# Kernel tuning notes

Hardware: AMD Instinct MI355X
Metric: run time of the kernel (lower is better)

The kernel has to match this reference:

```python
import jax, jax.numpy as jnp
import numpy as np

ALPHA = -100.0


def setup_inputs() -> dict:
    key = jax.random.key(0)
    k1, k2 = jax.random.split(key)
    input_seqs = jax.random.normal(k1, (512, 1024), dtype=jnp.float32)
    shapelets = jax.random.normal(k2, (100, 50), dtype=jnp.float32)
    return {"input_seqs": input_seqs, "shapelets": shapelets}


def reference(input_seqs, shapelets):
    """Sliding-window squared distance + softmin-weighted pooling.

    input_seqs: (n, Q) float
    shapelets : (K, L) float
    returns   : (n, K) float  -- softmin-pooled normalized sq. distance
    """
    n, Q = input_seqs.shape
    K, L = shapelets.shape
    J = Q - L  # original code uses Q - L (not Q - L + 1); kept faithful

    # ||x[j:j+L]||^2 for every window via cumulative sums (no explicit loop)
    csum = jnp.concatenate(
        [jnp.zeros((n, 1), input_seqs.dtype), jnp.cumsum(input_seqs * input_seqs, axis=1)],
        axis=1,
    )  # (n, Q+1)
    sq_win = csum[:, L:L + J] - csum[:, :J]  # (n, J)

    # cross term x[j:j+L] . s_k via windowed gather + small GEMM
    idx = jnp.arange(J)[:, None] + jnp.arange(L)[None, :]  # (J, L)
    windows = input_seqs[:, idx]  # (n, J, L)
    cross = jnp.einsum("njl,kl->njk", windows, shapelets)  # (n, J, K)

    s_sq = jnp.sum(shapelets * shapelets, axis=1)  # (K,)

    # D[i, j, k] = ||x_i[j:j+L] - s_k||^2 / L
    D = (sq_win[:, :, None] - 2.0 * cross + s_sq[None, None, :]) / L  # (n, J, K)

    # subtract per-(i,k) min over window positions (as in the original)
    Dm = D - jnp.min(D, axis=1, keepdims=True)

    # softmin-weighted average: sum_j Dm * exp(alpha*Dm) / sum_j exp(alpha*Dm)
    w = jnp.exp(ALPHA * Dm)  # stable: alpha<0 and Dm>=0 after min-shift
    M = jnp.sum(Dm * w, axis=1) / jnp.sum(w, axis=1)  # (n, K)
    return M
```

## Files before the change

### kernel.cpp

```cpp
#include <hip/hip_runtime.h>


#define N_SEQ   512
#define Q_LEN   1024
#define K_SH    100
#define L_SH    50
#define J_WIN   974
#define NTILE   7
#define MTILES  61
#define ALPHA_F (-100.0f)
#define SKIP_T  0.5f
#define RINV_L  0.02f
#define PAD_SQ  4e31f

#define CPR     1064

typedef short  short8 __attribute__((ext_vector_type(8)));
typedef float  f32x4  __attribute__((ext_vector_type(4)));
typedef unsigned int uintx4 __attribute__((ext_vector_type(4)));

union V8 { short8 s; uintx4 u; };

__device__ __forceinline__ unsigned int bf16h(float f) {
    unsigned int b = __float_as_uint(f);
    return (b + 0x7FFFu + ((b >> 16) & 1u)) >> 16;
}
__device__ __forceinline__ float bf16back(unsigned int h) {
    return __uint_as_float(h << 16);
}

__device__ __forceinline__ void merge_state(float& m, float& S, float& T,
                                            float m1, float S1, float T1) {
    const float mm = fminf(m, m1);
    const float e0 = __expf(ALPHA_F * (m  - mm));
    const float e1 = __expf(ALPHA_F * (m1 - mm));
    T = (T + (m - mm) * S) * e0 + (T1 + (m1 - mm) * S1) * e1;
    S = S * e0 + S1 * e1;
    m = mm;
}

__global__ __launch_bounds__(256, 2)
void softmin_mfma_kernel(const float* __restrict__ x,
                         const float* __restrict__ sh,
                         float* __restrict__ out) {
    __shared__ __align__(16) short cp[16 * CPR];
    __shared__ __align__(16) float lds_xf[1056];
    __shared__ __align__(16) float lds_sqw[984];
    __shared__ __align__(16) short bl_lds[64 * 120];
    __shared__ float red_buf[4][NTILE][16][3];

    const int i    = blockIdx.x;
    const int tid  = threadIdx.x;
    const int lane = tid & 63;
    const int w    = tid >> 6;
    const int g    = lane >> 4;
    const int bcol = lane & 15;

    short8 bh[NTILE][2];
    float  ssqv[NTILE];
    #pragma unroll
    for (int nt = 0; nt < NTILE; ++nt) {
        const int n = nt * 16 + bcol;
        float sv[16];
        #pragma unroll
        for (int e = 0; e < 16; ++e) sv[e] = 0.f;
        if (n < K_SH) {
            const float* srow = sh + n * L_SH;
            const float2* p0 = (const float2*)(srow + 8 * g);
            #pragma unroll
            for (int q = 0; q < 4; ++q) { float2 v = p0[q]; sv[2*q] = v.x; sv[2*q+1] = v.y; }
            if (g < 2) {
                const float2* p1 = (const float2*)(srow + 32 + 8 * g);
                #pragma unroll
                for (int q = 0; q < 4; ++q) { float2 v = p1[q]; sv[8+2*q] = v.x; sv[9+2*q] = v.y; }
            } else if (g == 2) {
                float2 v = *(const float2*)(srow + 48);
                sv[8] = v.x; sv[9] = v.y;
            }
        }
        float sq = 0.f;
        #pragma unroll
        for (int e = 0; e < 16; ++e) sq = fmaf(sv[e], sv[e], sq);
        sq += __shfl_xor(sq, 16);
        sq += __shfl_xor(sq, 32);
        ssqv[nt] = sq;

        unsigned int hb[16];
        #pragma unroll
        for (int e = 0; e < 16; ++e) hb[e] = bf16h(sv[e]);
        V8 h0, h1;
        h0.u = uintx4{hb[0]|(hb[1]<<16),  hb[2]|(hb[3]<<16),  hb[4]|(hb[5]<<16),  hb[6]|(hb[7]<<16)};
        h1.u = uintx4{hb[8]|(hb[9]<<16),  hb[10]|(hb[11]<<16),hb[12]|(hb[13]<<16),hb[14]|(hb[15]<<16)};
        bh[nt][0] = h0.s; bh[nt][1] = h1.s;

        if (tid < 64) {
            unsigned int lb[16];
            #pragma unroll
            for (int e = 0; e < 16; ++e) lb[e] = bf16h(sv[e] - bf16back(hb[e]));
            *(uintx4*)&bl_lds[lane*120 + nt*16] =
                uintx4{lb[0]|(lb[1]<<16),  lb[2]|(lb[3]<<16),  lb[4]|(lb[5]<<16),  lb[6]|(lb[7]<<16)};
            *(uintx4*)&bl_lds[lane*120 + nt*16 + 8] =
                uintx4{lb[8]|(lb[9]<<16),  lb[10]|(lb[11]<<16),lb[12]|(lb[13]<<16),lb[14]|(lb[15]<<16)};
        }
    }

    {
        const float4* gx = (const float4*)(x + (size_t)i * Q_LEN);
        float4* lx = (float4*)lds_xf;
        lx[tid] = gx[tid];
        if (tid < 8) lx[256 + tid] = make_float4(0.f, 0.f, 0.f, 0.f);
    }
    __syncthreads();

    if (tid < 246) {
        const float4* xf4 = (const float4*)lds_xf;
        float r0, r1, r2, r3;
        if (tid < 244) {
            float v[56];
            #pragma unroll
            for (int q = 0; q < 14; ++q) {
                float4 a = xf4[tid + q];
                v[4*q] = a.x; v[4*q+1] = a.y; v[4*q+2] = a.z; v[4*q+3] = a.w;
            }
            float s0 = 0.f;
            #pragma unroll
            for (int l = 0; l < L_SH; ++l) s0 = fmaf(v[l], v[l], s0);
            float s1 = fmaf(v[50], v[50], s0 - v[0]*v[0]);
            float s2 = fmaf(v[51], v[51], s1 - v[1]*v[1]);
            float s3 = fmaf(v[52], v[52], s2 - v[2]*v[2]);
            r0 = s0; r1 = s1; r2 = s2; r3 = s3;
            if (4*tid + 2 >= J_WIN) r2 = PAD_SQ;
            if (4*tid + 3 >= J_WIN) r3 = PAD_SQ;
        } else {
            r0 = r1 = r2 = r3 = PAD_SQ;
        }
        *(float4*)&lds_sqw[4*tid] = make_float4(r0, r1, r2, r3);
    }

    if (tid < 132) {
        const float4* xf4 = (const float4*)lds_xf;
        float4 a = xf4[2*tid], b = xf4[2*tid + 1];
        float xv[8] = {a.x, a.y, a.z, a.w, b.x, b.y, b.z, b.w};
        unsigned int hh[8], rr[8];
        #pragma unroll
        for (int e = 0; e < 8; ++e) {
            hh[e] = bf16h(xv[e]);
            rr[e] = bf16h(xv[e] - bf16back(hh[e]));
        }
        *(uintx4*)&cp[8*tid] =
            uintx4{hh[0]|(hh[1]<<16), hh[2]|(hh[3]<<16), hh[4]|(hh[5]<<16), hh[6]|(hh[7]<<16)};
        *(uintx4*)&cp[CPR + 8*tid] =
            uintx4{rr[0]|(rr[1]<<16), rr[2]|(rr[3]<<16), rr[4]|(rr[5]<<16), rr[6]|(rr[7]<<16)};
    }
    __syncthreads();

    for (int un = tid; un < 262; un += 256) {
        const int half = un & 1, blk = un >> 1;
        const uintx4 A  = *(const uintx4*)&cp[half*CPR + 8*blk];
        const uintx4 B4 = *(const uintx4*)&cp[half*CPR + 8*blk + 8];
        unsigned int s[8] = {A[0], A[1], A[2], A[3], B4[0], B4[1], B4[2], B4[3]};
        #pragma unroll
        for (int r = 1; r < 8; ++r) {
            const int p = r >> 1;
            unsigned int o[4];
            if ((r & 1) == 0) {
                #pragma unroll
                for (int e = 0; e < 4; ++e) o[e] = s[p + e];
            } else {
                #pragma unroll
                for (int e = 0; e < 4; ++e) o[e] = (s[p + e] >> 16) | (s[p + e + 1] << 16);
            }
            *(uintx4*)&cp[(2*r + half)*CPR + 8*blk] = uintx4{o[0], o[1], o[2], o[3]};
        }
    }
    __syncthreads();

    const int r7       = lane & 7;
    const int lane_off = 8 * ((lane >> 3) & 1) + 8 * g;
    const int abase0   = (2 * r7) * CPR + lane_off;

    float stM[NTILE], stS[NTILE], stT[NTILE];
    #pragma unroll
    for (int nt = 0; nt < NTILE; ++nt) { stM[nt] = 1e30f; stS[nt] = 0.f; stT[nt] = 0.f; }

    for (int mt = w; mt < MTILES; mt += 4) {
        const int j0 = mt << 4;
        const int ae = abase0 + j0;
        const short8 ah0 = *(const short8*)&cp[ae];
        const short8 ah1 = *(const short8*)&cp[ae + 32];
        const short8 al0 = *(const short8*)&cp[ae + CPR];
        const short8 al1 = *(const short8*)&cp[ae + CPR + 32];
        const float4 sqv = *(const float4*)&lds_sqw[j0 + 4 * g];
        const float b0 = sqv.x * RINV_L, b1 = sqv.y * RINV_L,
                    b2 = sqv.z * RINV_L, b3 = sqv.w * RINV_L;

        #pragma unroll
        for (int nt = 0; nt < NTILE; ++nt) {
            const short8 bl0 = *(const short8*)&bl_lds[lane*120 + nt*16];
            const short8 bl1 = *(const short8*)&bl_lds[lane*120 + nt*16 + 8];
            f32x4 acc = {0.f, 0.f, 0.f, 0.f};
            acc = __builtin_amdgcn_mfma_f32_16x16x32_bf16(ah0, bh[nt][0], acc, 0, 0, 0);
            acc = __builtin_amdgcn_mfma_f32_16x16x32_bf16(ah1, bh[nt][1], acc, 0, 0, 0);
            acc = __builtin_amdgcn_mfma_f32_16x16x32_bf16(al0, bh[nt][0], acc, 0, 0, 0);
            acc = __builtin_amdgcn_mfma_f32_16x16x32_bf16(al1, bh[nt][1], acc, 0, 0, 0);
            acc = __builtin_amdgcn_mfma_f32_16x16x32_bf16(ah0, bl0,       acc, 0, 0, 0);
            acc = __builtin_amdgcn_mfma_f32_16x16x32_bf16(ah1, bl1,       acc, 0, 0, 0);

            const float tb = ssqv[nt] * RINV_L;
            const float dv0 = fmaf(acc[0], -2.f * RINV_L, tb + b0);
            const float dv1 = fmaf(acc[1], -2.f * RINV_L, tb + b1);
            const float dv2 = fmaf(acc[2], -2.f * RINV_L, tb + b2);
            const float dv3 = fmaf(acc[3], -2.f * RINV_L, tb + b3);
            const float cmin = fminf(fminf(dv0, dv1), fminf(dv2, dv3));
            if (cmin < stM[nt] + SKIP_T) {
                float m2 = stM[nt], S2 = stS[nt], T2 = stT[nt];
                const float nm = fminf(m2, cmin);
                const float sc = __expf(ALPHA_F * (m2 - nm));
                T2 = (T2 + (m2 - nm) * S2) * sc;
                S2 = S2 * sc;
                m2 = nm;
                { const float t = dv0 - m2; const float wg = __expf(ALPHA_F * t); S2 += wg; T2 = fmaf(t, wg, T2); }
                { const float t = dv1 - m2; const float wg = __expf(ALPHA_F * t); S2 += wg; T2 = fmaf(t, wg, T2); }
                { const float t = dv2 - m2; const float wg = __expf(ALPHA_F * t); S2 += wg; T2 = fmaf(t, wg, T2); }
                { const float t = dv3 - m2; const float wg = __expf(ALPHA_F * t); S2 += wg; T2 = fmaf(t, wg, T2); }
                stM[nt] = m2; stS[nt] = S2; stT[nt] = T2;
            }
        }
    }

    #pragma unroll
    for (int nt = 0; nt < NTILE; ++nt) {
        float m = stM[nt], S = stS[nt], T = stT[nt];
        #pragma unroll
        for (int msk = 16; msk <= 32; msk <<= 1) {
            const float m1 = __shfl_xor(m, msk);
            const float S1 = __shfl_xor(S, msk);
            const float T1 = __shfl_xor(T, msk);
            merge_state(m, S, T, m1, S1, T1);
        }
        if (lane < 16) {
            red_buf[w][nt][lane][0] = m;
            red_buf[w][nt][lane][1] = S;
            red_buf[w][nt][lane][2] = T;
        }
    }
    __syncthreads();

    if (tid < NTILE * 16) {
        const int nt = tid >> 4, kk = tid & 15;
        float m = red_buf[0][nt][kk][0], S = red_buf[0][nt][kk][1], T = red_buf[0][nt][kk][2];
        #pragma unroll
        for (int ww = 1; ww < 4; ++ww)
            merge_state(m, S, T, red_buf[ww][nt][kk][0], red_buf[ww][nt][kk][1], red_buf[ww][nt][kk][2]);
        const int k = nt * 16 + kk;
        if (k < K_SH) out[(size_t)i * K_SH + k] = T / S;
    }
}

extern "C" void kernel_launch(void* const* d_in, const int* in_sizes, int n_in,
                              void* d_out, int out_size, void* d_ws, size_t ws_size,
                              hipStream_t stream) {
    const float* x  = (const float*)d_in[0];
    const float* sh = (const float*)d_in[1];
    float* out = (float*)d_out;

    softmin_mfma_kernel<<<N_SEQ, 256, 0, stream>>>(x, sh, out);
}
```

Measured before the change: 88.04 us.

## Use two-pass softmin with precomputed min and 512-thread blocks

Replaces the online softmin (running min with rescaling and a data-dependent skip branch) with two passes. A cheap first pass uses only the high-part bf16 MFMAs to find an approximate per-shapelet minimum. A second full-precision pass then accumulates plain exp2 sums against that fixed minimum, and the result is corrected by the difference between the exact and approximate minima. It also drops the shapelet squared-norm term, since it cancels after the min-shift, and doubles the block to 8 waves. The cost is an extra MFMA pass and a mostly exp-dense inner loop. If the approximate minimum is off, the exponent offset can underflow the weights.

```diff
diff --git a/kernel.cpp b/kernel.cpp
--- a/kernel.cpp
+++ b/kernel.cpp
@@ -8,12 +8,13 @@
 #define J_WIN   974
 #define NTILE   7
 #define MTILES  61
-#define ALPHA_F (-100.0f)
-#define SKIP_T  0.5f
+#define NWAVE   8
 #define RINV_L  0.02f
 #define PAD_SQ  4e31f
+#define CQ      (-2.8853900817779268f)
 
 #define CPR     1064
+#define BLSTR   120
 
 typedef short  short8 __attribute__((ext_vector_type(8)));
 typedef float  f32x4  __attribute__((ext_vector_type(4)));
@@ -29,25 +30,14 @@
     return __uint_as_float(h << 16);
 }
 
-__device__ __forceinline__ void merge_state(float& m, float& S, float& T,
-                                            float m1, float S1, float T1) {
-    const float mm = fminf(m, m1);
-    const float e0 = __expf(ALPHA_F * (m  - mm));
-    const float e1 = __expf(ALPHA_F * (m1 - mm));
-    T = (T + (m - mm) * S) * e0 + (T1 + (m1 - mm) * S1) * e1;
-    S = S * e0 + S1 * e1;
-    m = mm;
-}
-
-__global__ __launch_bounds__(256, 2)
+__global__ __launch_bounds__(512, 4)
 void softmin_mfma_kernel(const float* __restrict__ x,
                          const float* __restrict__ sh,
                          float* __restrict__ out) {
     __shared__ __align__(16) short cp[16 * CPR];
     __shared__ __align__(16) float lds_xf[1056];
     __shared__ __align__(16) float lds_sqw[984];
-    __shared__ __align__(16) short bl_lds[64 * 120];
-    __shared__ float red_buf[4][NTILE][16][3];
+    __shared__ __align__(16) short bl_lds[64 * BLSTR];
 
     const int i    = blockIdx.x;
     const int tid  = threadIdx.x;
@@ -57,7 +47,6 @@
     const int bcol = lane & 15;
 
     short8 bh[NTILE][2];
-    float  ssqv[NTILE];
     #pragma unroll
     for (int nt = 0; nt < NTILE; ++nt) {
         const int n = nt * 16 + bcol;
@@ -78,13 +67,6 @@
                 sv[8] = v.x; sv[9] = v.y;
             }
         }
-        float sq = 0.f;
-        #pragma unroll
-        for (int e = 0; e < 16; ++e) sq = fmaf(sv[e], sv[e], sq);
-        sq += __shfl_xor(sq, 16);
-        sq += __shfl_xor(sq, 32);
-        ssqv[nt] = sq;
-
         unsigned int hb[16];
         #pragma unroll
         for (int e = 0; e < 16; ++e) hb[e] = bf16h(sv[e]);
@@ -97,9 +79,9 @@
             unsigned int lb[16];
             #pragma unroll
             for (int e = 0; e < 16; ++e) lb[e] = bf16h(sv[e] - bf16back(hb[e]));
-            *(uintx4*)&bl_lds[lane*120 + nt*16] =
+            *(uintx4*)&bl_lds[lane*BLSTR + nt*16] =
                 uintx4{lb[0]|(lb[1]<<16),  lb[2]|(lb[3]<<16),  lb[4]|(lb[5]<<16),  lb[6]|(lb[7]<<16)};
-            *(uintx4*)&bl_lds[lane*120 + nt*16 + 8] =
+            *(uintx4*)&bl_lds[lane*BLSTR + nt*16 + 8] =
                 uintx4{lb[8]|(lb[9]<<16),  lb[10]|(lb[11]<<16),lb[12]|(lb[13]<<16),lb[14]|(lb[15]<<16)};
         }
     }
@@ -107,8 +89,8 @@
     {
         const float4* gx = (const float4*)(x + (size_t)i * Q_LEN);
         float4* lx = (float4*)lds_xf;
-        lx[tid] = gx[tid];
-        if (tid < 8) lx[256 + tid] = make_float4(0.f, 0.f, 0.f, 0.f);
+        if (tid < 256) lx[tid] = gx[tid];
+        if (tid < 8)   lx[256 + tid] = make_float4(0.f, 0.f, 0.f, 0.f);
     }
     __syncthreads();
 
@@ -154,8 +136,8 @@
     }
     __syncthreads();
 
-    for (int un = tid; un < 262; un += 256) {
-        const int half = un & 1, blk = un >> 1;
+    if (tid < 262) {
+        const int half = tid & 1, blk = tid >> 1;
         const uintx4 A  = *(const uintx4*)&cp[half*CPR + 8*blk];
         const uintx4 B4 = *(const uintx4*)&cp[half*CPR + 8*blk + 8];
         unsigned int s[8] = {A[0], A[1], A[2], A[3], B4[0], B4[1], B4[2], B4[3]};
@@ -179,11 +161,56 @@
     const int lane_off = 8 * ((lane >> 3) & 1) + 8 * g;
     const int abase0   = (2 * r7) * CPR + lane_off;
 
-    float stM[NTILE], stS[NTILE], stT[NTILE];
-    #pragma unroll
-    for (int nt = 0; nt < NTILE; ++nt) { stM[nt] = 1e30f; stS[nt] = 0.f; stT[nt] = 0.f; }
-
-    for (int mt = w; mt < MTILES; mt += 4) {
+    float mreg[NTILE];
+    #pragma unroll
+    for (int nt = 0; nt < NTILE; ++nt) mreg[nt] = 1e30f;
+
+    for (int mt = w; mt < MTILES; mt += NWAVE) {
+        const int j0 = mt << 4;
+        const int ae = abase0 + j0;
+        const short8 ah0 = *(const short8*)&cp[ae];
+        const short8 ah1 = *(const short8*)&cp[ae + 32];
+        const float4 sqv = *(const float4*)&lds_sqw[j0 + 4 * g];
+
+        #pragma unroll
+        for (int nt = 0; nt < NTILE; ++nt) {
+            f32x4 acc = {0.f, 0.f, 0.f, 0.f};
+            acc = __builtin_amdgcn_mfma_f32_16x16x32_bf16(ah0, bh[nt][0], acc, 0, 0, 0);
+            acc = __builtin_amdgcn_mfma_f32_16x16x32_bf16(ah1, bh[nt][1], acc, 0, 0, 0);
+            const float q0 = fmaf(acc[0], -2.f, sqv.x);
+            const float q1 = fmaf(acc[1], -2.f, sqv.y);
+            const float q2 = fmaf(acc[2], -2.f, sqv.z);
+            const float q3 = fmaf(acc[3], -2.f, sqv.w);
+            mreg[nt] = fminf(mreg[nt], fminf(fminf(q0, q1), fminf(q2, q3)));
+        }
+    }
+
+    float* wred = lds_xf;
+    float* gm   = lds_xf + 896;
+    #pragma unroll
+    for (int nt = 0; nt < NTILE; ++nt) {
+        float mm = mreg[nt];
+        mm = fminf(mm, __shfl_xor(mm, 16));
+        mm = fminf(mm, __shfl_xor(mm, 32));
+        if (lane < 16) wred[(w * NTILE + nt) * 16 + lane] = mm;
+    }
+    __syncthreads();
+    if (tid < NTILE * 16) {
+        float v = wred[tid];
+        #pragma unroll
+        for (int ww = 1; ww < NWAVE; ++ww) v = fminf(v, wred[ww * 112 + tid]);
+        gm[tid] = v;
+    }
+    __syncthreads();
+    float mqa[NTILE];
+    #pragma unroll
+    for (int nt = 0; nt < NTILE; ++nt) mqa[nt] = gm[nt * 16 + bcol];
+
+    float Sv[NTILE], Tv[NTILE], mq2[NTILE];
+    #pragma unroll
+    for (int nt = 0; nt < NTILE; ++nt) { Sv[nt] = 0.f; Tv[nt] = 0.f; mq2[nt] = 1e30f; }
+
+    for (int mt = w; mt < MTILES; mt += NWAVE) {
         const int j0 = mt << 4;
         const int ae = abase0 + j0;
         const short8 ah0 = *(const short8*)&cp[ae];
@@ -191,13 +218,11 @@
         const short8 al0 = *(const short8*)&cp[ae + CPR];
         const short8 al1 = *(const short8*)&cp[ae + CPR + 32];
         const float4 sqv = *(const float4*)&lds_sqw[j0 + 4 * g];
-        const float b0 = sqv.x * RINV_L, b1 = sqv.y * RINV_L,
-                    b2 = sqv.z * RINV_L, b3 = sqv.w * RINV_L;
 
         #pragma unroll
         for (int nt = 0; nt < NTILE; ++nt) {
-            const short8 bl0 = *(const short8*)&bl_lds[lane*120 + nt*16];
-            const short8 bl1 = *(const short8*)&bl_lds[lane*120 + nt*16 + 8];
+            const short8 bl0 = *(const short8*)&bl_lds[lane*BLSTR + nt*16];
+            const short8 bl1 = *(const short8*)&bl_lds[lane*BLSTR + nt*16 + 8];
             f32x4 acc = {0.f, 0.f, 0.f, 0.f};
             acc = __builtin_amdgcn_mfma_f32_16x16x32_bf16(ah0, bh[nt][0], acc, 0, 0, 0);
             acc = __builtin_amdgcn_mfma_f32_16x16x32_bf16(ah1, bh[nt][1], acc, 0, 0, 0);
@@ -206,54 +231,64 @@
             acc = __builtin_amdgcn_mfma_f32_16x16x32_bf16(ah0, bl0,       acc, 0, 0, 0);
             acc = __builtin_amdgcn_mfma_f32_16x16x32_bf16(ah1, bl1,       acc, 0, 0, 0);
 
-            const float tb = ssqv[nt] * RINV_L;
-            const float dv0 = fmaf(acc[0], -2.f * RINV_L, tb + b0);
-            const float dv1 = fmaf(acc[1], -2.f * RINV_L, tb + b1);
-            const float dv2 = fmaf(acc[2], -2.f * RINV_L, tb + b2);
-            const float dv3 = fmaf(acc[3], -2.f * RINV_L, tb + b3);
-            const float cmin = fminf(fminf(dv0, dv1), fminf(dv2, dv3));
-            if (cmin < stM[nt] + SKIP_T) {
-                float m2 = stM[nt], S2 = stS[nt], T2 = stT[nt];
-                const float nm = fminf(m2, cmin);
-                const float sc = __expf(ALPHA_F * (m2 - nm));
-                T2 = (T2 + (m2 - nm) * S2) * sc;
-                S2 = S2 * sc;
-                m2 = nm;
-                { const float t = dv0 - m2; const float wg = __expf(ALPHA_F * t); S2 += wg; T2 = fmaf(t, wg, T2); }
-                { const float t = dv1 - m2; const float wg = __expf(ALPHA_F * t); S2 += wg; T2 = fmaf(t, wg, T2); }
-                { const float t = dv2 - m2; const float wg = __expf(ALPHA_F * t); S2 += wg; T2 = fmaf(t, wg, T2); }
-                { const float t = dv3 - m2; const float wg = __expf(ALPHA_F * t); S2 += wg; T2 = fmaf(t, wg, T2); }
-                stM[nt] = m2; stS[nt] = S2; stT[nt] = T2;
-            }
-        }
-    }
-
+            const float q0 = fmaf(acc[0], -2.f, sqv.x);
+            const float q1 = fmaf(acc[1], -2.f, sqv.y);
+            const float q2 = fmaf(acc[2], -2.f, sqv.z);
+            const float q3 = fmaf(acc[3], -2.f, sqv.w);
+            mq2[nt] = fminf(mq2[nt], fminf(fminf(q0, q1), fminf(q2, q3)));
+
+            const float mq = mqa[nt];
+            const float t0 = q0 - mq, t1 = q1 - mq, t2 = q2 - mq, t3 = q3 - mq;
+            const float w0 = exp2f(t0 * CQ);
+            const float w1 = exp2f(t1 * CQ);
+            const float w2 = exp2f(t2 * CQ);
+            const float w3 = exp2f(t3 * CQ);
+            Sv[nt] += (w0 + w1) + (w2 + w3);
+            float tv = Tv[nt];
+            tv = fmaf(t0, w0, tv);
+            tv = fmaf(t1, w1, tv);
+            tv = fmaf(t2, w2, tv);
+            tv = fmaf(t3, w3, tv);
+            Tv[nt] = tv;
+        }
+    }
+
+    float rm[NTILE], rS[NTILE], rT[NTILE];
     #pragma unroll
     for (int nt = 0; nt < NTILE; ++nt) {
-        float m = stM[nt], S = stS[nt], T = stT[nt];
-        #pragma unroll
-        for (int msk = 16; msk <= 32; msk <<= 1) {
-            const float m1 = __shfl_xor(m, msk);
-            const float S1 = __shfl_xor(S, msk);
-            const float T1 = __shfl_xor(T, msk);
-            merge_state(m, S, T, m1, S1, T1);
-        }
+        float a = mq2[nt], s = Sv[nt], t = Tv[nt];
+        a = fminf(a, __shfl_xor(a, 16));
+        a = fminf(a, __shfl_xor(a, 32));
+        s += __shfl_xor(s, 16);  s += __shfl_xor(s, 32);
+        t += __shfl_xor(t, 16);  t += __shfl_xor(t, 32);
+        rm[nt] = a; rS[nt] = s; rT[nt] = t;
+    }
+    __syncthreads();
+    float* redS = (float*)cp;
+    float* redT = redS + 896;
+    #pragma unroll
+    for (int nt = 0; nt < NTILE; ++nt) {
         if (lane < 16) {
-            red_buf[w][nt][lane][0] = m;
-            red_buf[w][nt][lane][1] = S;
-            red_buf[w][nt][lane][2] = T;
+            const int idx = (w * NTILE + nt) * 16 + lane;
+            wred[idx] = rm[nt];
+            redS[idx] = rS[nt];
+            redT[idx] = rT[nt];
         }
     }
     __syncthreads();
 
     if (tid < NTILE * 16) {
+        float mfin = wred[tid], Sf = redS[tid], Tf = redT[tid];
+        #pragma unroll
+        for (int ww = 1; ww < NWAVE; ++ww) {
+            mfin = fminf(mfin, wred[ww * 112 + tid]);
+            Sf += redS[ww * 112 + tid];
+            Tf += redT[ww * 112 + tid];
+        }
         const int nt = tid >> 4, kk = tid & 15;
-        float m = red_buf[0][nt][kk][0], S = red_buf[0][nt][kk][1], T = red_buf[0][nt][kk][2];
-        #pragma unroll
-        for (int ww = 1; ww < 4; ++ww)
-            merge_state(m, S, T, red_buf[ww][nt][kk][0], red_buf[ww][nt][kk][1], red_buf[ww][nt][kk][2]);
         const int k = nt * 16 + kk;
-        if (k < K_SH) out[(size_t)i * K_SH + k] = T / S;
+        const float delta = mfin - gm[tid];
+        if (k < K_SH) out[(size_t)i * K_SH + k] = (Tf / Sf - delta) * RINV_L;
     }
 }
 
@@ -264,5 +299,5 @@
     const float* sh = (const float*)d_in[1];
     float* out = (float*)d_out;
 
-    softmin_mfma_kernel<<<N_SEQ, 256, 0, stream>>>(x, sh, out);
+    softmin_mfma_kernel<<<N_SEQ, 512, 0, stream>>>(x, sh, out);
 }
```

New measurement: 162.1 us. 1.84x slower.
